# Performance work log

Hardware: AMD Instinct MI355X
Metric: run time of the kernel (lower is better)

## Reference

```python
import math
import jax, jax.numpy as jnp
import numpy as np

INVALID_VALUE = -0.1  # ChannelPositions.INVALID_VALUE sentinel
POS_DIM = 288
MARGIN = 0.2
N_FREQS = 12  # int(sqrt(POS_DIM // 2))


def fourier_emb(positions):
    # positions: [..., 2] in [0, 1]; returns [..., POS_DIM]
    freqs = jnp.arange(N_FREQS, dtype=positions.dtype)
    width = 1.0 + 2.0 * MARGIN
    pos = positions + MARGIN
    p = (2.0 * math.pi / width) * freqs  # [K]
    # loc[..., i, j] = pos_x * p[i] + pos_y * p[j]
    loc = pos[..., None, None, 0] * p[:, None] + pos[..., None, None, 1] * p[None, :]
    loc = loc.reshape(*positions.shape[:-1], N_FREQS * N_FREQS)  # [..., 144]
    return jnp.concatenate([jnp.cos(loc), jnp.sin(loc)], axis=-1)  # [..., 288]


def setup_inputs() -> dict:
    key = jax.random.key(0)
    k1, k2, k3, k4 = jax.random.split(key, 4)
    B, C, T = 128, 273, 2048
    chout, n_subjects = 270, 200
    meg = jax.random.normal(k1, (B, C, T), dtype=jnp.float32)
    positions = jax.random.uniform(k2, (B, C, 2), dtype=jnp.float32)
    subject_ids = jax.random.randint(k3, (B,), 0, n_subjects)
    heads = jax.random.normal(k4, (n_subjects, chout, POS_DIM), dtype=jnp.float32) / math.sqrt(POS_DIM)
    return {"meg": meg, "positions": positions, "subject_ids": subject_ids, "heads": heads}


def reference(meg, positions, subject_ids, heads):
    # meg: [B,C,T], positions: [B,C,2], subject_ids: [B], heads: [S,O,D]
    emb = fourier_emb(positions)            # [B,C,D]
    h = heads[subject_ids]                  # per-subject gather -> [B,O,D]
    scores = jnp.einsum('bcd,bod->boc', emb, h)  # [B,O,C]
    invalid = jnp.all(positions == INVALID_VALUE, axis=-1)  # [B,C]
    scores = jnp.where(invalid[:, None, :], -jnp.inf, scores)
    weights = jax.nn.softmax(scores, axis=2)     # over channels C
    out = jnp.einsum('bct,boc->bot', meg, weights)  # [B,O,T]
    return out
```

## Files before the change

kernel.cpp:

```cpp
#include <hip/hip_runtime.h>
#include <math.h>

#define B_ 128
#define C_ 273
#define T_ 2048
#define O_ 270
#define D_ 288
#define OP_ 288
#define CP_ 384
#define KP_ 288

typedef __attribute__((ext_vector_type(8))) short short8;
typedef __attribute__((ext_vector_type(4))) float f32x4;

__device__ inline ushort f2bf(float f) {
    uint u = __float_as_uint(f);
    return (ushort)((u + 0x7FFFu + ((u >> 16) & 1u)) >> 16);
}
__device__ inline uint pack2bf(float lo, float hi) {
    return (uint)f2bf(lo) | ((uint)f2bf(hi) << 16);
}

__global__ __launch_bounds__(256) void k_emb(const float* __restrict__ pos,
                                             ushort* __restrict__ emb) {
    int idx = blockIdx.x * 256 + threadIdx.x;
    const int total = B_ * CP_ * 144;
    if (idx >= total) return;
    int bc = idx / 144;
    int k  = idx - bc * 144;
    int b  = bc / CP_;
    int c  = bc - b * CP_;
    ushort* row = emb + ((size_t)b * CP_ + c) * D_;
    if (c >= C_) { row[k] = 0; row[144 + k] = 0; return; }
    int i = k / 12, j = k - i * 12;
    float px = pos[((size_t)b * C_ + c) * 2 + 0] + 0.2f;
    float py = pos[((size_t)b * C_ + c) * 2 + 1] + 0.2f;
    const float w0 = 4.48798950512827605f;
    float loc = px * (w0 * (float)i) + py * (w0 * (float)j);
    float s, cc;
    __sincosf(loc, &s, &cc);
    row[k]       = f2bf(cc);
    row[144 + k] = f2bf(s);
}

__global__ __launch_bounds__(256) void k_gather(const float* __restrict__ heads,
                                                const int* __restrict__ sids,
                                                ushort* __restrict__ hb) {
    int idx = blockIdx.x * 256 + threadIdx.x;
    const int total = B_ * OP_ * (D_ / 8);
    if (idx >= total) return;
    int d8 = (idx % 36) * 8;
    int t  = idx / 36;
    int o  = t % OP_;
    int b  = t / OP_;
    uint4 outv = make_uint4(0, 0, 0, 0);
    if (o < O_) {
        int sid = sids[b];
        const float* src = heads + ((size_t)sid * O_ + o) * D_ + d8;
        float4 v0 = *(const float4*)src;
        float4 v1 = *(const float4*)(src + 4);
        outv.x = pack2bf(v0.x, v0.y); outv.y = pack2bf(v0.z, v0.w);
        outv.z = pack2bf(v1.x, v1.y); outv.w = pack2bf(v1.z, v1.w);
    }
    *(uint4*)(hb + ((size_t)b * OP_ + o) * D_ + d8) = outv;
}

__device__ inline void stage_ab(const ushort* __restrict__ A0,
                                const ushort* __restrict__ B0,
                                uint* buf, int wid, int lane) {
    for (int ch = wid; ch < 14; ch += 4) {
        bool isA = ch < 6;
        int slotb = (isA ? ch : ch - 6) << 6;
        int slot  = slotb + lane;
        const ushort* g = (isA ? A0 : B0) + (size_t)(slot >> 2) * KP_ + ((slot & 3) << 3);
        uint* dst = buf + (isA ? (slotb << 2) : (1536 + (slotb << 2)));
        __builtin_amdgcn_global_load_lds(
            (const __attribute__((address_space(1))) uint*)g,
            (__attribute__((address_space(3))) uint*)dst, 16, 0, 0);
    }
}

__global__ __launch_bounds__(256) void k_scores(const ushort* __restrict__ hb,
                                                const ushort* __restrict__ emb,
                                                float* __restrict__ scores) {
    __shared__ uint LdsU[2 * 3584];
    int b  = blockIdx.z;
    int o0 = blockIdx.y * 96;
    int n0 = blockIdx.x * 128;
    int tid = threadIdx.x;
    int wid = tid >> 6, lane = tid & 63;
    int wm = wid >> 1, wn = wid & 1;
    int lm = lane & 15, lq = lane >> 4;
    const ushort* Ab = hb  + ((size_t)b * OP_ + o0) * D_;
    const ushort* Bb = emb + ((size_t)b * CP_ + n0) * D_;
    f32x4 acc[3][4];
    #pragma unroll
    for (int i = 0; i < 3; ++i)
        #pragma unroll
        for (int j = 0; j < 4; ++j) { f32x4 z = {0.f, 0.f, 0.f, 0.f}; acc[i][j] = z; }

    auto compute = [&](int cb) {
        const ushort* As = (const ushort*)(LdsU + cb * 3584);
        const ushort* Bs = (const ushort*)(LdsU + cb * 3584 + 1536);
        short8 a[3], bv[4];
        #pragma unroll
        for (int fm = 0; fm < 3; ++fm)
            a[fm] = *(const short8*)(As + (wm * 48 + fm * 16 + lm) * 32 + lq * 8);
        #pragma unroll
        for (int fn = 0; fn < 4; ++fn)
            bv[fn] = *(const short8*)(Bs + (wn * 64 + fn * 16 + lm) * 32 + lq * 8);
        #pragma unroll
        for (int fm = 0; fm < 3; ++fm)
            #pragma unroll
            for (int fn = 0; fn < 4; ++fn)
                acc[fm][fn] = __builtin_amdgcn_mfma_f32_16x16x32_bf16(a[fm], bv[fn], acc[fm][fn], 0, 0, 0);
    };

    int cur = 0;
    stage_ab(Ab, Bb, LdsU, wid, lane);
    __syncthreads();
    for (int k = 0; k < 8; ++k) {
        int nk = (k + 1) * 32;
        stage_ab(Ab + nk, Bb + nk, LdsU + (cur ^ 1) * 3584, wid, lane);
        compute(cur);
        __syncthreads();
        cur ^= 1;
    }
    compute(cur);

    #pragma unroll
    for (int fm = 0; fm < 3; ++fm) {
        int obase = o0 + wm * 48 + fm * 16 + lq * 4;
        #pragma unroll
        for (int fn = 0; fn < 4; ++fn) {
            int c = n0 + wn * 64 + fn * 16 + lm;
            if (c >= C_) continue;
            #pragma unroll
            for (int r = 0; r < 4; ++r) {
                int o = obase + r;
                if (o < O_) scores[((size_t)b * O_ + o) * C_ + c] = acc[fm][fn][r];
            }
        }
    }
}

__global__ __launch_bounds__(256) void k_softmax(const float* __restrict__ scores,
                                                 const float* __restrict__ pos,
                                                 ushort* __restrict__ wbf) {
    int wave = threadIdx.x >> 6, lane = threadIdx.x & 63;
    int row = blockIdx.x * 4 + wave;
    if (row >= B_ * OP_) return;
    int b = row / OP_, o = row - b * OP_;
    ushort* wrow = wbf + ((size_t)b * OP_ + o) * KP_;
    if (o >= O_) {
        #pragma unroll
        for (int ch = 0; ch < 5; ++ch) { int c = lane + ch * 64; if (c < KP_) wrow[c] = 0; }
        return;
    }
    const float* srow = scores + ((size_t)b * O_ + o) * C_;
    const float* prow = pos + (size_t)b * C_ * 2;
    float v[5];
    float m = -INFINITY;
    #pragma unroll
    for (int ch = 0; ch < 5; ++ch) {
        int c = lane + ch * 64;
        float s = -INFINITY;
        if (c < C_) {
            s = srow[c];
            float px = prow[c * 2], py = prow[c * 2 + 1];
            if (px == -0.1f && py == -0.1f) s = -INFINITY;
        }
        v[ch] = s;
        m = fmaxf(m, s);
    }
    #pragma unroll
    for (int off = 32; off; off >>= 1) m = fmaxf(m, __shfl_xor(m, off, 64));
    float sum = 0.f;
    #pragma unroll
    for (int ch = 0; ch < 5; ++ch) {
        v[ch] = __expf(v[ch] - m);
        if (lane + ch * 64 < C_) sum += v[ch];
    }
    #pragma unroll
    for (int off = 32; off; off >>= 1) sum += __shfl_xor(sum, off, 64);
    float inv = 1.0f / sum;
    #pragma unroll
    for (int ch = 0; ch < 5; ++ch) {
        int c = lane + ch * 64;
        if (c < C_) wrow[c] = f2bf(v[ch] * inv);
        else if (c < KP_) wrow[c] = 0;
    }
}

__global__ __launch_bounds__(256) void k_megT(const float* __restrict__ meg,
                                              ushort* __restrict__ megT) {
    __shared__ float lds[64 * 65];
    int b  = blockIdx.z;
    int t0 = blockIdx.x * 64;
    int c0 = blockIdx.y * 64;
    int tid = threadIdx.x;
    const float* Mb = meg + (size_t)b * C_ * T_;
    #pragma unroll
    for (int i = 0; i < 4; ++i) {
        int slot = tid + i * 256;
        int r = slot >> 4, q = slot & 15;
        float4 v = make_float4(0.f, 0.f, 0.f, 0.f);
        if (c0 + r < C_) v = *(const float4*)(Mb + (size_t)(c0 + r) * T_ + t0 + q * 4);
        lds[r * 65 + q * 4 + 0] = v.x;
        lds[r * 65 + q * 4 + 1] = v.y;
        lds[r * 65 + q * 4 + 2] = v.z;
        lds[r * 65 + q * 4 + 3] = v.w;
    }
    __syncthreads();
    ushort* Tb = megT + (size_t)b * T_ * KP_;
    #pragma unroll
    for (int i = 0; i < 2; ++i) {
        int slot = tid + i * 256;
        int t = slot >> 3, co = (slot & 7) * 8;
        int c = c0 + co;
        if (c >= KP_) continue;
        uint4 w;
        w.x = pack2bf(lds[(co + 0) * 65 + t], lds[(co + 1) * 65 + t]);
        w.y = pack2bf(lds[(co + 2) * 65 + t], lds[(co + 3) * 65 + t]);
        w.z = pack2bf(lds[(co + 4) * 65 + t], lds[(co + 5) * 65 + t]);
        w.w = pack2bf(lds[(co + 6) * 65 + t], lds[(co + 7) * 65 + t]);
        *(uint4*)(Tb + (size_t)(t0 + t) * KP_ + c) = w;
    }
}

__global__ __launch_bounds__(256) void k_out(const ushort* __restrict__ megT,
                                             const ushort* __restrict__ wbf,
                                             float* __restrict__ out) {
    __shared__ uint LdsU[2 * 3584];
    int b  = blockIdx.z;
    int o0 = blockIdx.y * 96;
    int t0 = blockIdx.x * 128;
    int tid = threadIdx.x;
    int wid = tid >> 6, lane = tid & 63;
    int wm = wid >> 1, wn = wid & 1;
    int lm = lane & 15, lq = lane >> 4;
    const ushort* Ab = wbf  + ((size_t)b * OP_ + o0) * KP_;
    const ushort* Bb = megT + ((size_t)b * T_ + t0) * KP_;
    f32x4 acc[3][4];
    #pragma unroll
    for (int i = 0; i < 3; ++i)
        #pragma unroll
        for (int j = 0; j < 4; ++j) { f32x4 z = {0.f, 0.f, 0.f, 0.f}; acc[i][j] = z; }

    auto compute = [&](int cb) {
        const ushort* As = (const ushort*)(LdsU + cb * 3584);
        const ushort* Bs = (const ushort*)(LdsU + cb * 3584 + 1536);
        short8 a[3], bv[4];
        #pragma unroll
        for (int fm = 0; fm < 3; ++fm)
            a[fm] = *(const short8*)(As + (wm * 48 + fm * 16 + lm) * 32 + lq * 8);
        #pragma unroll
        for (int fn = 0; fn < 4; ++fn)
            bv[fn] = *(const short8*)(Bs + (wn * 64 + fn * 16 + lm) * 32 + lq * 8);
        #pragma unroll
        for (int fm = 0; fm < 3; ++fm)
            #pragma unroll
            for (int fn = 0; fn < 4; ++fn)
                acc[fm][fn] = __builtin_amdgcn_mfma_f32_16x16x32_bf16(a[fm], bv[fn], acc[fm][fn], 0, 0, 0);
    };

    int cur = 0;
    stage_ab(Ab, Bb, LdsU, wid, lane);
    __syncthreads();
    for (int k = 0; k < 8; ++k) {
        int nk = (k + 1) * 32;
        stage_ab(Ab + nk, Bb + nk, LdsU + (cur ^ 1) * 3584, wid, lane);
        compute(cur);
        __syncthreads();
        cur ^= 1;
    }
    compute(cur);

    #pragma unroll
    for (int fm = 0; fm < 3; ++fm) {
        int obase = o0 + wm * 48 + fm * 16 + lq * 4;
        #pragma unroll
        for (int fn = 0; fn < 4; ++fn) {
            int t = t0 + wn * 64 + fn * 16 + lm;
            #pragma unroll
            for (int r = 0; r < 4; ++r) {
                int o = obase + r;
                if (o < O_) out[((size_t)b * O_ + o) * T_ + t] = acc[fm][fn][r];
            }
        }
    }
}

__global__ __launch_bounds__(256) void k_out_fused(const float* __restrict__ meg,
                                                   const ushort* __restrict__ wbf,
                                                   float* __restrict__ out) {
    __shared__ uint AsU[96 * 16];
    __shared__ uint BsU[128 * 16];
    int b  = blockIdx.z;
    int o0 = blockIdx.y * 96;
    int t0 = blockIdx.x * 128;
    int tid = threadIdx.x;
    int wid = tid >> 6, lane = tid & 63;
    int wm = wid >> 1, wn = wid & 1;
    int lm = lane & 15, lq = lane >> 4;
    const ushort* Ab = wbf + (size_t)b * OP_ * KP_;
    const float*  Mb = meg + (size_t)b * C_ * T_;
    f32x4 acc[3][4];
    #pragma unroll
    for (int i = 0; i < 3; ++i)
        #pragma unroll
        for (int j = 0; j < 4; ++j) { f32x4 z = {0.f, 0.f, 0.f, 0.f}; acc[i][j] = z; }

    int cpair = tid & 15;
    int tq0   = tid >> 4;

    for (int k0 = 0; k0 < KP_; k0 += 32) {
        {
            int row = tid >> 2, ch = tid & 3;
            uint4 v = *(const uint4*)(Ab + (size_t)(o0 + row) * KP_ + k0 + ch * 8);
            *(uint4*)&AsU[tid * 4] = v;
            if (tid < 128) {
                int s2 = 256 + tid, row2 = s2 >> 2, ch2 = s2 & 3;
                uint4 v2 = *(const uint4*)(Ab + (size_t)(o0 + row2) * KP_ + k0 + ch2 * 8);
                *(uint4*)&AsU[s2 * 4] = v2;
            }
        }
        #pragma unroll
        for (int it = 0; it < 2; ++it) {
            int tqq = tq0 + it * 16;
            int c   = k0 + cpair * 2;
            int t   = tqq * 4;
            float4 v0 = make_float4(0.f, 0.f, 0.f, 0.f);
            float4 v1 = make_float4(0.f, 0.f, 0.f, 0.f);
            if (c < C_)     v0 = *(const float4*)(Mb + (size_t)c * T_ + t0 + t);
            if (c + 1 < C_) v1 = *(const float4*)(Mb + (size_t)(c + 1) * T_ + t0 + t);
            BsU[(t + 0) * 16 + cpair] = pack2bf(v0.x, v1.x);
            BsU[(t + 1) * 16 + cpair] = pack2bf(v0.y, v1.y);
            BsU[(t + 2) * 16 + cpair] = pack2bf(v0.z, v1.z);
            BsU[(t + 3) * 16 + cpair] = pack2bf(v0.w, v1.w);
        }
        __syncthreads();
        short8 a[3], bb[4];
        #pragma unroll
        for (int fm = 0; fm < 3; ++fm)
            a[fm] = *(short8*)((ushort*)AsU + (wm * 48 + fm * 16 + lm) * 32 + lq * 8);
        #pragma unroll
        for (int fn = 0; fn < 4; ++fn)
            bb[fn] = *(short8*)((ushort*)BsU + (wn * 64 + fn * 16 + lm) * 32 + lq * 8);
        #pragma unroll
        for (int fm = 0; fm < 3; ++fm)
            #pragma unroll
            for (int fn = 0; fn < 4; ++fn)
                acc[fm][fn] = __builtin_amdgcn_mfma_f32_16x16x32_bf16(a[fm], bb[fn], acc[fm][fn], 0, 0, 0);
        __syncthreads();
    }
    #pragma unroll
    for (int fm = 0; fm < 3; ++fm) {
        int obase = o0 + wm * 48 + fm * 16 + lq * 4;
        #pragma unroll
        for (int fn = 0; fn < 4; ++fn) {
            int t = t0 + wn * 64 + fn * 16 + lm;
            #pragma unroll
            for (int r = 0; r < 4; ++r) {
                int o = obase + r;
                if (o < O_) out[((size_t)b * O_ + o) * T_ + t] = acc[fm][fn][r];
            }
        }
    }
}

extern "C" void kernel_launch(void* const* d_in, const int* in_sizes, int n_in,
                              void* d_out, int out_size, void* d_ws, size_t ws_size,
                              hipStream_t stream) {
    const float* meg   = (const float*)d_in[0];
    const float* pos   = (const float*)d_in[1];
    const int*   sids  = (const int*)d_in[2];
    const float* heads = (const float*)d_in[3];
    float* out = (float*)d_out;

    const size_t embElems = (size_t)B_ * CP_ * D_;
    const size_t hbElems  = (size_t)B_ * OP_ * D_;
    ushort* emb = (ushort*)d_ws;
    ushort* wbf = emb;
    ushort* hb  = emb + embElems;
    float* scores = (float*)(hb + hbElems);
    ushort* megT  = hb;
    const size_t need_new = embElems * 2 + (size_t)B_ * T_ * KP_ * 2;

    k_emb<<<(B_ * CP_ * 144 + 255) / 256, 256, 0, stream>>>(pos, emb);
    k_gather<<<(B_ * OP_ * 36 + 255) / 256, 256, 0, stream>>>(heads, sids, hb);
    k_scores<<<dim3(3, 3, B_), 256, 0, stream>>>(hb, emb, scores);
    k_softmax<<<(B_ * OP_ + 3) / 4, 256, 0, stream>>>(scores, pos, wbf);
    if (ws_size >= need_new) {
        k_megT<<<dim3(T_ / 64, 5, B_), 256, 0, stream>>>(meg, megT);
        k_out<<<dim3(T_ / 128, 3, B_), 256, 0, stream>>>(megT, wbf, out);
    } else {
        k_out_fused<<<dim3(T_ / 128, 3, B_), 256, 0, stream>>>(meg, wbf, out);
    }
}
```

Before: 708.6 us.

## Fuse scores and softmax, widen out tiles, chunk megT, add XCD swizzle

Scores GEMM and softmax merge into one kernel that holds a full 96x288 score tile in registers, applies the invalid-channel mask as a bias and does the row max and sum through shuffles and LDS. This removes the fp32 scores round trip through memory. The channel padding drops from 384 to 288. k_out now computes every output row per block so each megT tile is loaded once, block indices are remapped across XCDs, and megT is built in batch chunks sized to the workspace instead of falling back to a fused path. The larger accumulator arrays raise register pressure and may lower occupancy.

New measurement: 698.7 us. Within noise of the previous version (-1.4%).

```diff
diff --git a/kernel.cpp b/kernel.cpp
--- a/kernel.cpp
+++ b/kernel.cpp
@@ -7,7 +7,7 @@
 #define O_ 270
 #define D_ 288
 #define OP_ 288
-#define CP_ 384
+#define CP_ 288
 #define KP_ 288
 
 typedef __attribute__((ext_vector_type(8))) short short8;
@@ -19,6 +19,11 @@
 }
 __device__ inline uint pack2bf(float lo, float hi) {
     return (uint)f2bf(lo) | ((uint)f2bf(hi) << 16);
+}
+
+__device__ inline int xcd_swz(int h, int nwg) {
+    int q = nwg >> 3, r = nwg & 7, x = h & 7, s = h >> 3;
+    return (x < r ? x * (q + 1) : r * (q + 1) + (x - r) * q) + s;
 }
 
 __global__ __launch_bounds__(256) void k_emb(const float* __restrict__ pos,
@@ -65,141 +70,161 @@
     *(uint4*)(hb + ((size_t)b * OP_ + o) * D_ + d8) = outv;
 }
 
-__device__ inline void stage_ab(const ushort* __restrict__ A0,
-                                const ushort* __restrict__ B0,
-                                uint* buf, int wid, int lane) {
-    for (int ch = wid; ch < 14; ch += 4) {
-        bool isA = ch < 6;
-        int slotb = (isA ? ch : ch - 6) << 6;
-        int slot  = slotb + lane;
+template<int ACH, int BCH, int BBASE>
+__device__ inline void stage2(const ushort* __restrict__ A0,
+                              const ushort* __restrict__ B0,
+                              uint* buf, int wid, int lane) {
+    for (int ch = wid; ch < ACH + BCH; ch += 4) {
+        bool isA = ch < ACH;
+        int cb = isA ? ch : ch - ACH;
+        int slot = (cb << 6) + lane;
         const ushort* g = (isA ? A0 : B0) + (size_t)(slot >> 2) * KP_ + ((slot & 3) << 3);
-        uint* dst = buf + (isA ? (slotb << 2) : (1536 + (slotb << 2)));
+        uint* dst = buf + (isA ? 0 : BBASE) + (slot << 2);
         __builtin_amdgcn_global_load_lds(
             (const __attribute__((address_space(1))) uint*)g,
             (__attribute__((address_space(3))) uint*)dst, 16, 0, 0);
     }
 }
 
-__global__ __launch_bounds__(256) void k_scores(const ushort* __restrict__ hb,
-                                                const ushort* __restrict__ emb,
-                                                float* __restrict__ scores) {
-    __shared__ uint LdsU[2 * 3584];
-    int b  = blockIdx.z;
-    int o0 = blockIdx.y * 96;
-    int n0 = blockIdx.x * 128;
+__global__ __launch_bounds__(256) void k_fused(const ushort* __restrict__ hb,
+                                               const ushort* __restrict__ emb,
+                                               const float* __restrict__ pos,
+                                               ushort* __restrict__ wbf) {
+    __shared__ uint LdsU[2 * 6144];
+    __shared__ float red[2][2][96];
+    int d  = xcd_swz(blockIdx.x, 3 * B_);
+    int ob = d % 3, b = d / 3;
+    int o0 = ob * 96;
     int tid = threadIdx.x;
     int wid = tid >> 6, lane = tid & 63;
     int wm = wid >> 1, wn = wid & 1;
     int lm = lane & 15, lq = lane >> 4;
     const ushort* Ab = hb  + ((size_t)b * OP_ + o0) * D_;
-    const ushort* Bb = emb + ((size_t)b * CP_ + n0) * D_;
-    f32x4 acc[3][4];
+    const ushort* Bb = emb + (size_t)b * CP_ * D_;
+
+    const float* prow = pos + (size_t)b * C_ * 2;
+    float bias[9];
+    #pragma unroll
+    for (int fn = 0; fn < 9; ++fn) {
+        int c = wn * 144 + fn * 16 + lm;
+        float bv = -INFINITY;
+        if (c < C_) {
+            float px = prow[c * 2], py = prow[c * 2 + 1];
+            bv = (px == -0.1f && py == -0.1f) ? -INFINITY : 0.0f;
+        }
+        bias[fn] = bv;
+    }
+
+    f32x4 acc[3][9];
     #pragma unroll
     for (int i = 0; i < 3; ++i)
         #pragma unroll
-        for (int j = 0; j < 4; ++j) { f32x4 z = {0.f, 0.f, 0.f, 0.f}; acc[i][j] = z; }
+        for (int j = 0; j < 9; ++j) { f32x4 z = {0.f, 0.f, 0.f, 0.f}; acc[i][j] = z; }
 
     auto compute = [&](int cb) {
-        const ushort* As = (const ushort*)(LdsU + cb * 3584);
-        const ushort* Bs = (const ushort*)(LdsU + cb * 3584 + 1536);
-        short8 a[3], bv[4];
+        const ushort* As = (const ushort*)(LdsU + cb * 6144);
+        const ushort* Bs = (const ushort*)(LdsU + cb * 6144 + 1536);
+        short8 av[3];
         #pragma unroll
         for (int fm = 0; fm < 3; ++fm)
-            a[fm] = *(const short8*)(As + (wm * 48 + fm * 16 + lm) * 32 + lq * 8);
-        #pragma unroll
-        for (int fn = 0; fn < 4; ++fn)
-            bv[fn] = *(const short8*)(Bs + (wn * 64 + fn * 16 + lm) * 32 + lq * 8);
-        #pragma unroll
-        for (int fm = 0; fm < 3; ++fm)
-            #pragma unroll
-            for (int fn = 0; fn < 4; ++fn)
-                acc[fm][fn] = __builtin_amdgcn_mfma_f32_16x16x32_bf16(a[fm], bv[fn], acc[fm][fn], 0, 0, 0);
+            av[fm] = *(const short8*)(As + (wm * 48 + fm * 16 + lm) * 32 + lq * 8);
+        #pragma unroll
+        for (int fn = 0; fn < 9; ++fn) {
+            short8 bv = *(const short8*)(Bs + (wn * 144 + fn * 16 + lm) * 32 + lq * 8);
+            #pragma unroll
+            for (int fm = 0; fm < 3; ++fm)
+                acc[fm][fn] = __builtin_amdgcn_mfma_f32_16x16x32_bf16(av[fm], bv, acc[fm][fn], 0, 0, 0);
+        }
     };
 
     int cur = 0;
-    stage_ab(Ab, Bb, LdsU, wid, lane);
+    stage2<6, 18, 1536>(Ab, Bb, LdsU, wid, lane);
     __syncthreads();
     for (int k = 0; k < 8; ++k) {
         int nk = (k + 1) * 32;
-        stage_ab(Ab + nk, Bb + nk, LdsU + (cur ^ 1) * 3584, wid, lane);
+        stage2<6, 18, 1536>(Ab + nk, Bb + nk, LdsU + (cur ^ 1) * 6144, wid, lane);
         compute(cur);
         __syncthreads();
         cur ^= 1;
     }
     compute(cur);
 
-    #pragma unroll
-    for (int fm = 0; fm < 3; ++fm) {
-        int obase = o0 + wm * 48 + fm * 16 + lq * 4;
-        #pragma unroll
-        for (int fn = 0; fn < 4; ++fn) {
-            int c = n0 + wn * 64 + fn * 16 + lm;
-            if (c >= C_) continue;
+    float mx[3][4];
+    #pragma unroll
+    for (int fm = 0; fm < 3; ++fm)
+        #pragma unroll
+        for (int r = 0; r < 4; ++r) {
+            float m = -INFINITY;
+            #pragma unroll
+            for (int fn = 0; fn < 9; ++fn) m = fmaxf(m, acc[fm][fn][r] + bias[fn]);
+            #pragma unroll
+            for (int off = 1; off < 16; off <<= 1) m = fmaxf(m, __shfl_xor(m, off, 64));
+            mx[fm][r] = m;
+        }
+    if (lm == 0) {
+        #pragma unroll
+        for (int fm = 0; fm < 3; ++fm)
+            #pragma unroll
+            for (int r = 0; r < 4; ++r)
+                red[0][wn][wm * 48 + fm * 16 + lq * 4 + r] = mx[fm][r];
+    }
+    __syncthreads();
+    float Mv[3][4], sm[3][4];
+    #pragma unroll
+    for (int fm = 0; fm < 3; ++fm)
+        #pragma unroll
+        for (int r = 0; r < 4; ++r) {
+            int row = wm * 48 + fm * 16 + lq * 4 + r;
+            Mv[fm][r] = fmaxf(red[0][0][row], red[0][1][row]);
+            sm[fm][r] = 0.f;
+        }
+    #pragma unroll
+    for (int fm = 0; fm < 3; ++fm)
+        #pragma unroll
+        for (int fn = 0; fn < 9; ++fn)
             #pragma unroll
             for (int r = 0; r < 4; ++r) {
-                int o = obase + r;
-                if (o < O_) scores[((size_t)b * O_ + o) * C_ + c] = acc[fm][fn][r];
+                float e = __expf(acc[fm][fn][r] + bias[fn] - Mv[fm][r]);
+                acc[fm][fn][r] = e;
+                sm[fm][r] += e;
             }
-        }
-    }
-}
-
-__global__ __launch_bounds__(256) void k_softmax(const float* __restrict__ scores,
-                                                 const float* __restrict__ pos,
-                                                 ushort* __restrict__ wbf) {
-    int wave = threadIdx.x >> 6, lane = threadIdx.x & 63;
-    int row = blockIdx.x * 4 + wave;
-    if (row >= B_ * OP_) return;
-    int b = row / OP_, o = row - b * OP_;
-    ushort* wrow = wbf + ((size_t)b * OP_ + o) * KP_;
-    if (o >= O_) {
-        #pragma unroll
-        for (int ch = 0; ch < 5; ++ch) { int c = lane + ch * 64; if (c < KP_) wrow[c] = 0; }
-        return;
-    }
-    const float* srow = scores + ((size_t)b * O_ + o) * C_;
-    const float* prow = pos + (size_t)b * C_ * 2;
-    float v[5];
-    float m = -INFINITY;
-    #pragma unroll
-    for (int ch = 0; ch < 5; ++ch) {
-        int c = lane + ch * 64;
-        float s = -INFINITY;
-        if (c < C_) {
-            s = srow[c];
-            float px = prow[c * 2], py = prow[c * 2 + 1];
-            if (px == -0.1f && py == -0.1f) s = -INFINITY;
-        }
-        v[ch] = s;
-        m = fmaxf(m, s);
-    }
-    #pragma unroll
-    for (int off = 32; off; off >>= 1) m = fmaxf(m, __shfl_xor(m, off, 64));
-    float sum = 0.f;
-    #pragma unroll
-    for (int ch = 0; ch < 5; ++ch) {
-        v[ch] = __expf(v[ch] - m);
-        if (lane + ch * 64 < C_) sum += v[ch];
-    }
-    #pragma unroll
-    for (int off = 32; off; off >>= 1) sum += __shfl_xor(sum, off, 64);
-    float inv = 1.0f / sum;
-    #pragma unroll
-    for (int ch = 0; ch < 5; ++ch) {
-        int c = lane + ch * 64;
-        if (c < C_) wrow[c] = f2bf(v[ch] * inv);
-        else if (c < KP_) wrow[c] = 0;
-    }
+    #pragma unroll
+    for (int fm = 0; fm < 3; ++fm)
+        #pragma unroll
+        for (int r = 0; r < 4; ++r) {
+            #pragma unroll
+            for (int off = 1; off < 16; off <<= 1) sm[fm][r] += __shfl_xor(sm[fm][r], off, 64);
+        }
+    if (lm == 0) {
+        #pragma unroll
+        for (int fm = 0; fm < 3; ++fm)
+            #pragma unroll
+            for (int r = 0; r < 4; ++r)
+                red[1][wn][wm * 48 + fm * 16 + lq * 4 + r] = sm[fm][r];
+    }
+    __syncthreads();
+    ushort* Wb = wbf + (size_t)b * OP_ * KP_;
+    #pragma unroll
+    for (int fm = 0; fm < 3; ++fm)
+        #pragma unroll
+        for (int r = 0; r < 4; ++r) {
+            int row = wm * 48 + fm * 16 + lq * 4 + r;
+            float inv = 1.0f / (red[1][0][row] + red[1][1][row]);
+            ushort* wr = Wb + (size_t)(o0 + row) * KP_ + wn * 144 + lm;
+            #pragma unroll
+            for (int fn = 0; fn < 9; ++fn)
+                wr[fn * 16] = f2bf(acc[fm][fn][r] * inv);
+        }
 }
 
 __global__ __launch_bounds__(256) void k_megT(const float* __restrict__ meg,
-                                              ushort* __restrict__ megT) {
+                                              ushort* __restrict__ megT, int b0) {
     __shared__ float lds[64 * 65];
-    int b  = blockIdx.z;
+    int bl = blockIdx.z;
     int t0 = blockIdx.x * 64;
     int c0 = blockIdx.y * 64;
     int tid = threadIdx.x;
-    const float* Mb = meg + (size_t)b * C_ * T_;
+    const float* Mb = meg + (size_t)(b0 + bl) * C_ * T_;
     #pragma unroll
     for (int i = 0; i < 4; ++i) {
         int slot = tid + i * 256;
@@ -212,7 +237,7 @@
         lds[r * 65 + q * 4 + 3] = v.w;
     }
     __syncthreads();
-    ushort* Tb = megT + (size_t)b * T_ * KP_;
+    ushort* Tb = megT + (size_t)bl * T_ * KP_;
     #pragma unroll
     for (int i = 0; i < 2; ++i) {
         int slot = tid + i * 256;
@@ -230,46 +255,47 @@
 
 __global__ __launch_bounds__(256) void k_out(const ushort* __restrict__ megT,
                                              const ushort* __restrict__ wbf,
-                                             float* __restrict__ out) {
-    __shared__ uint LdsU[2 * 3584];
-    int b  = blockIdx.z;
-    int o0 = blockIdx.y * 96;
-    int t0 = blockIdx.x * 128;
+                                             float* __restrict__ out,
+                                             int b0, int nb) {
+    __shared__ uint LdsU[2 * 6656];
+    int d  = xcd_swz(blockIdx.x, 16 * nb);
+    int tb = d & 15, bl = d >> 4;
+    int b  = b0 + bl;
+    int t0 = tb * 128;
     int tid = threadIdx.x;
     int wid = tid >> 6, lane = tid & 63;
     int wm = wid >> 1, wn = wid & 1;
     int lm = lane & 15, lq = lane >> 4;
-    const ushort* Ab = wbf  + ((size_t)b * OP_ + o0) * KP_;
-    const ushort* Bb = megT + ((size_t)b * T_ + t0) * KP_;
-    f32x4 acc[3][4];
-    #pragma unroll
-    for (int i = 0; i < 3; ++i)
+    const ushort* Ab = wbf  + (size_t)b * OP_ * KP_;
+    const ushort* Bb = megT + ((size_t)bl * T_ + t0) * KP_;
+    f32x4 acc[9][4];
+    #pragma unroll
+    for (int i = 0; i < 9; ++i)
         #pragma unroll
         for (int j = 0; j < 4; ++j) { f32x4 z = {0.f, 0.f, 0.f, 0.f}; acc[i][j] = z; }
 
     auto compute = [&](int cb) {
-        const ushort* As = (const ushort*)(LdsU + cb * 3584);
-        const ushort* Bs = (const ushort*)(LdsU + cb * 3584 + 1536);
-        short8 a[3], bv[4];
-        #pragma unroll
-        for (int fm = 0; fm < 3; ++fm)
-            a[fm] = *(const short8*)(As + (wm * 48 + fm * 16 + lm) * 32 + lq * 8);
+        const ushort* As = (const ushort*)(LdsU + cb * 6656);
+        const ushort* Bs = (const ushort*)(LdsU + cb * 6656 + 4608);
+        short8 bv[4];
         #pragma unroll
         for (int fn = 0; fn < 4; ++fn)
             bv[fn] = *(const short8*)(Bs + (wn * 64 + fn * 16 + lm) * 32 + lq * 8);
         #pragma unroll
-        for (int fm = 0; fm < 3; ++fm)
+        for (int fm = 0; fm < 9; ++fm) {
+            short8 av = *(const short8*)(As + (wm * 144 + fm * 16 + lm) * 32 + lq * 8);
             #pragma unroll
             for (int fn = 0; fn < 4; ++fn)
-                acc[fm][fn] = __builtin_amdgcn_mfma_f32_16x16x32_bf16(a[fm], bv[fn], acc[fm][fn], 0, 0, 0);
+                acc[fm][fn] = __builtin_amdgcn_mfma_f32_16x16x32_bf16(av, bv[fn], acc[fm][fn], 0, 0, 0);
+        }
     };
 
     int cur = 0;
-    stage_ab(Ab, Bb, LdsU, wid, lane);
+    stage2<18, 8, 4608>(Ab, Bb, LdsU, wid, lane);
     __syncthreads();
     for (int k = 0; k < 8; ++k) {
         int nk = (k + 1) * 32;
-        stage_ab(Ab + nk, Bb + nk, LdsU + (cur ^ 1) * 3584, wid, lane);
+        stage2<18, 8, 4608>(Ab + nk, Bb + nk, LdsU + (cur ^ 1) * 6656, wid, lane);
         compute(cur);
         __syncthreads();
         cur ^= 1;
@@ -277,86 +303,8 @@
     compute(cur);
 
     #pragma unroll
-    for (int fm = 0; fm < 3; ++fm) {
-        int obase = o0 + wm * 48 + fm * 16 + lq * 4;
-        #pragma unroll
-        for (int fn = 0; fn < 4; ++fn) {
-            int t = t0 + wn * 64 + fn * 16 + lm;
-            #pragma unroll
-            for (int r = 0; r < 4; ++r) {
-                int o = obase + r;
-                if (o < O_) out[((size_t)b * O_ + o) * T_ + t] = acc[fm][fn][r];
-            }
-        }
-    }
-}
-
-__global__ __launch_bounds__(256) void k_out_fused(const float* __restrict__ meg,
-                                                   const ushort* __restrict__ wbf,
-                                                   float* __restrict__ out) {
-    __shared__ uint AsU[96 * 16];
-    __shared__ uint BsU[128 * 16];
-    int b  = blockIdx.z;
-    int o0 = blockIdx.y * 96;
-    int t0 = blockIdx.x * 128;
-    int tid = threadIdx.x;
-    int wid = tid >> 6, lane = tid & 63;
-    int wm = wid >> 1, wn = wid & 1;
-    int lm = lane & 15, lq = lane >> 4;
-    const ushort* Ab = wbf + (size_t)b * OP_ * KP_;
-    const float*  Mb = meg + (size_t)b * C_ * T_;
-    f32x4 acc[3][4];
-    #pragma unroll
-    for (int i = 0; i < 3; ++i)
-        #pragma unroll
-        for (int j = 0; j < 4; ++j) { f32x4 z = {0.f, 0.f, 0.f, 0.f}; acc[i][j] = z; }
-
-    int cpair = tid & 15;
-    int tq0   = tid >> 4;
-
-    for (int k0 = 0; k0 < KP_; k0 += 32) {
-        {
-            int row = tid >> 2, ch = tid & 3;
-            uint4 v = *(const uint4*)(Ab + (size_t)(o0 + row) * KP_ + k0 + ch * 8);
-            *(uint4*)&AsU[tid * 4] = v;
-            if (tid < 128) {
-                int s2 = 256 + tid, row2 = s2 >> 2, ch2 = s2 & 3;
-                uint4 v2 = *(const uint4*)(Ab + (size_t)(o0 + row2) * KP_ + k0 + ch2 * 8);
-                *(uint4*)&AsU[s2 * 4] = v2;
-            }
-        }
-        #pragma unroll
-        for (int it = 0; it < 2; ++it) {
-            int tqq = tq0 + it * 16;
-            int c   = k0 + cpair * 2;
-            int t   = tqq * 4;
-            float4 v0 = make_float4(0.f, 0.f, 0.f, 0.f);
-            float4 v1 = make_float4(0.f, 0.f, 0.f, 0.f);
-            if (c < C_)     v0 = *(const float4*)(Mb + (size_t)c * T_ + t0 + t);
-            if (c + 1 < C_) v1 = *(const float4*)(Mb + (size_t)(c + 1) * T_ + t0 + t);
-            BsU[(t + 0) * 16 + cpair] = pack2bf(v0.x, v1.x);
-            BsU[(t + 1) * 16 + cpair] = pack2bf(v0.y, v1.y);
-            BsU[(t + 2) * 16 + cpair] = pack2bf(v0.z, v1.z);
-            BsU[(t + 3) * 16 + cpair] = pack2bf(v0.w, v1.w);
-        }
-        __syncthreads();
-        short8 a[3], bb[4];
-        #pragma unroll
-        for (int fm = 0; fm < 3; ++fm)
-            a[fm] = *(short8*)((ushort*)AsU + (wm * 48 + fm * 16 + lm) * 32 + lq * 8);
-        #pragma unroll
-        for (int fn = 0; fn < 4; ++fn)
-            bb[fn] = *(short8*)((ushort*)BsU + (wn * 64 + fn * 16 + lm) * 32 + lq * 8);
-        #pragma unroll
-        for (int fm = 0; fm < 3; ++fm)
-            #pragma unroll
-            for (int fn = 0; fn < 4; ++fn)
-                acc[fm][fn] = __builtin_amdgcn_mfma_f32_16x16x32_bf16(a[fm], bb[fn], acc[fm][fn], 0, 0, 0);
-        __syncthreads();
-    }
-    #pragma unroll
-    for (int fm = 0; fm < 3; ++fm) {
-        int obase = o0 + wm * 48 + fm * 16 + lq * 4;
+    for (int fm = 0; fm < 9; ++fm) {
+        int obase = wm * 144 + fm * 16 + lq * 4;
         #pragma unroll
         for (int fn = 0; fn < 4; ++fn) {
             int t = t0 + wn * 64 + fn * 16 + lm;
@@ -378,23 +326,23 @@
     const float* heads = (const float*)d_in[3];
     float* out = (float*)d_out;
 
-    const size_t embElems = (size_t)B_ * CP_ * D_;
-    const size_t hbElems  = (size_t)B_ * OP_ * D_;
-    ushort* emb = (ushort*)d_ws;
-    ushort* wbf = emb;
-    ushort* hb  = emb + embElems;
-    float* scores = (float*)(hb + hbElems);
-    ushort* megT  = hb;
-    const size_t need_new = embElems * 2 + (size_t)B_ * T_ * KP_ * 2;
+    const size_t embE = (size_t)B_ * CP_ * D_;
+    ushort* emb  = (ushort*)d_ws;
+    ushort* hb   = emb + embE;
+    ushort* wbf  = hb + embE;
+    ushort* megT = wbf + embE;
+    const size_t perB = (size_t)T_ * KP_ * 2;
+    size_t avail = ws_size > 3 * embE * 2 ? ws_size - 3 * embE * 2 : 0;
+    int chunkB = (int)(avail / perB);
+    if (chunkB > B_) chunkB = B_;
+    if (chunkB < 1) chunkB = 1;
 
     k_emb<<<(B_ * CP_ * 144 + 255) / 256, 256, 0, stream>>>(pos, emb);
     k_gather<<<(B_ * OP_ * 36 + 255) / 256, 256, 0, stream>>>(heads, sids, hb);
-    k_scores<<<dim3(3, 3, B_), 256, 0, stream>>>(hb, emb, scores);
-    k_softmax<<<(B_ * OP_ + 3) / 4, 256, 0, stream>>>(scores, pos, wbf);
-    if (ws_size >= need_new) {
-        k_megT<<<dim3(T_ / 64, 5, B_), 256, 0, stream>>>(meg, megT);
-        k_out<<<dim3(T_ / 128, 3, B_), 256, 0, stream>>>(megT, wbf, out);
-    } else {
-        k_out_fused<<<dim3(T_ / 128, 3, B_), 256, 0, stream>>>(meg, wbf, out);
-    }
-}
+    k_fused<<<3 * B_, 256, 0, stream>>>(hb, emb, pos, wbf);
+    for (int b0 = 0; b0 < B_; b0 += chunkB) {
+        int nb = (B_ - b0 < chunkB) ? (B_ - b0) : chunkB;
+        k_megT<<<dim3(T_ / 64, 5, nb), 256, 0, stream>>>(meg, megT, b0);
+        k_out<<<16 * nb, 256, 0, stream>>>(megT, wbf, out, b0, nb);
+    }
+}
```
